# Kernel tuning notes

Hardware: AMD Instinct MI355X
Metric: run time of the kernel (lower is better)

Reference implementation:

```python
import jax, jax.numpy as jnp
import numpy as np

N_NODES = 100000
N_EDGES = 1600000
IN_C, HID_C, OUT_C = 128, 128, 64


def gcn_conv(x, src, dst, W, b, num_nodes):
    # PyG GCNConv: add self-loops, symmetric normalization, linear transform,
    # aggregate source features into targets.
    h = x @ W  # [N, C_out]
    loop = jnp.arange(num_nodes, dtype=src.dtype)
    s = jnp.concatenate([src, loop])
    d = jnp.concatenate([dst, loop])
    deg = jax.ops.segment_sum(jnp.ones_like(d, dtype=h.dtype), d, num_segments=num_nodes)
    inv_sqrt = jnp.where(deg > 0, jax.lax.rsqrt(deg), 0.0)
    norm = inv_sqrt[s] * inv_sqrt[d]  # [E+N]
    msgs = h[s] * norm[:, None]  # gather + scale
    out = jax.ops.segment_sum(msgs, d, num_segments=num_nodes)  # scatter-add
    return out + b


def setup_inputs() -> dict:
    key = jax.random.key(0)
    k1, k2, k3, k4 = jax.random.split(key, 4)
    x = jax.random.normal(k1, (N_NODES, IN_C), dtype=jnp.float32)
    edge_index = jax.random.randint(k2, (2, N_EDGES), 0, N_NODES, dtype=jnp.int64)
    W1 = jax.random.normal(k3, (IN_C, HID_C), dtype=jnp.float32) * (1.0 / np.sqrt(IN_C))
    b1 = jnp.zeros((HID_C,), dtype=jnp.float32)
    W2 = jax.random.normal(k4, (HID_C, OUT_C), dtype=jnp.float32) * (1.0 / np.sqrt(HID_C))
    b2 = jnp.zeros((OUT_C,), dtype=jnp.float32)
    return {"x": x, "edge_index": edge_index, "W1": W1, "b1": b1, "W2": W2, "b2": b2}


def reference(x, edge_index, W1, b1, W2, b2):
    num_nodes = x.shape[0]
    src, dst = edge_index[0], edge_index[1]  # PyG flow: source -> target
    h = gcn_conv(x, src, dst, W1, b1, num_nodes)
    h = jax.nn.relu(h)  # dropout is identity in eval mode
    out = gcn_conv(h, src, dst, W2, b2, num_nodes)
    return out
```

## Files before the change

kernel.cpp:

```cpp
#include <hip/hip_runtime.h>

#define IN_C 128
#define HID_C 128
#define OUT_C 64

#define BSPAN 256
#define BCAP  5120
#define NBMAX 512
#define ACHUNK 4096

typedef unsigned int uint32;
typedef unsigned short ushort16;
typedef _Float16 f16;
typedef f16   f16x8 __attribute__((ext_vector_type(8)));
typedef float f32x4 __attribute__((ext_vector_type(4)));


__device__ __forceinline__ ushort16 f2bf(float f) {
    union { float f; uint32 u; } v; v.f = f;
    uint32 r = v.u + 0x7FFFu + ((v.u >> 16) & 1u);
    return (ushort16)(r >> 16);
}

__device__ __forceinline__ void unpack2(uint32 u, float& f0, float& f1) {
    union { uint32 x; float f; } a, b;
    a.x = u << 16;
    b.x = u & 0xFFFF0000u;
    f0 = a.f; f1 = b.f;
}


__launch_bounds__(256)
__global__ void bin_edges_kernel(const int* __restrict__ src, const int* __restrict__ dst,
                                 int* __restrict__ bucketCur, uint32* __restrict__ binned,
                                 int E, int nbuck) {
    __shared__ int hist[NBMAX];
    __shared__ int base[NBMAX];
    const int tid = threadIdx.x;
    const int e0  = blockIdx.x * ACHUNK;

    for (int i = tid; i < NBMAX; i += 256) hist[i] = 0;
    __syncthreads();

    int d[16], s[16], rk[16];
#pragma unroll
    for (int j = 0; j < 16; j++) {
        int e = e0 + j * 256 + tid;
        if (e < E) {
            d[j] = dst[e];
            s[j] = src[e];
            rk[j] = atomicAdd(&hist[d[j] >> 8], 1);
        } else d[j] = -1;
    }
    __syncthreads();

    for (int b = tid; b < nbuck; b += 256) {
        int h = hist[b];
        base[b] = h ? atomicAdd(&bucketCur[b], h) : 0;
    }
    __syncthreads();

#pragma unroll
    for (int j = 0; j < 16; j++) {
        if (d[j] >= 0) {
            int b = d[j] >> 8;
            int pos = base[b] + rk[j];
            if (pos < BCAP)
                binned[(size_t)b * BCAP + pos] =
                    ((uint32)(d[j] & 255) << 17) | (uint32)s[j];
        }
    }
}


__launch_bounds__(256)
__global__ void bucket_csr_kernel(const uint32* __restrict__ binned,
                                  const int* __restrict__ bucketCur,
                                  int* __restrict__ csr_src, int* __restrict__ rowbeg,
                                  int* __restrict__ rowend, float* __restrict__ inv, int N) {
    constexpr int MAXIT = BCAP / 256;
    __shared__ int cnt[BSPAN];
    __shared__ int scn[BSPAN];
    __shared__ int excl[BSPAN];
    const int b   = blockIdx.x;
    const int tid = threadIdx.x;
    const int n0  = b * BSPAN;
    const int ne  = min(bucketCur[b], BCAP);
    const uint32* bp = binned + (size_t)b * BCAP;

    cnt[tid] = 0;
    __syncthreads();

    uint32 ebuf[MAXIT];
    int    rbuf[MAXIT];
    int nmine = 0;
    for (int i = tid; i < ne; i += 256) {
        uint32 e = bp[i];
        ebuf[nmine] = e;
        rbuf[nmine] = atomicAdd(&cnt[e >> 17], 1);
        nmine++;
    }
    __syncthreads();

    int v = cnt[tid];
    scn[tid] = v;
    __syncthreads();
    for (int off = 1; off < 256; off <<= 1) {
        int u = (tid >= off) ? scn[tid - off] : 0;
        __syncthreads();
        scn[tid] += u;
        __syncthreads();
    }
    int ex = scn[tid] - v;
    excl[tid] = ex;

    int n = n0 + tid;
    if (n < N) {
        int gb = b * BCAP + ex;
        rowbeg[n] = gb;
        rowend[n] = gb + v;
        inv[n] = rsqrtf((float)(v + 1));
    }
    __syncthreads();

    for (int j = 0; j < nmine; j++) {
        uint32 e = ebuf[j];
        csr_src[(size_t)b * BCAP + excl[e >> 17] + rbuf[j]] = (int)(e & 0x1FFFFu);
    }
}


template <int C>
__device__ __forceinline__ void wprep_one(const float* __restrict__ W, f16* __restrict__ Wf, int t) {
    constexpr int NCT = C / 16;
    int lane = t & 63;
    int ctkc = t >> 6;
    int ct = ctkc % NCT, kc = ctkc / NCT;
    int kbase = kc * 32 + (lane >> 4) * 8;
    int col   = ct * 16 + (lane & 15);
    f16 v[8];
#pragma unroll
    for (int j = 0; j < 8; j++) v[j] = (f16)W[(size_t)(kbase + j) * C + col];
    *(uint4*)(Wf + (size_t)t * 8) = *(const uint4*)v;
}

__global__ void wprep_both(const float* __restrict__ W1, f16* __restrict__ Wf1,
                           const float* __restrict__ W2, f16* __restrict__ Wf2) {
    constexpr int T1 = 4 * (HID_C / 16) * 64;
    constexpr int T2 = 4 * (OUT_C / 16) * 64;
    int t = blockIdx.x * 256 + threadIdx.x;
    if (t < T1)            wprep_one<HID_C>(W1, Wf1, t);
    else if (t < T1 + T2)  wprep_one<OUT_C>(W2, Wf2, t - T1);
}


template <int C, bool AF16>
__launch_bounds__(256)
__global__ void mfma_gemm(const void* __restrict__ Xv, const f16* __restrict__ Wf,
                          const float* __restrict__ inv, ushort16* __restrict__ outb, int N) {
    constexpr int NCT = C / 16;
    __shared__ __align__(16) f16 As[4 * 4 * 64 * 8];
    __shared__ __align__(16) f16 Bs[4 * NCT * 64 * 8];

    const int tid  = threadIdx.x;
    const int lane = tid & 63;
    const int w    = tid >> 6;
    const int row0 = blockIdx.x * 64;

    {
        constexpr int TOT = 4 * NCT * 64 * 8;
        const uint4* src = (const uint4*)Wf;
        uint4* dst = (uint4*)Bs;
#pragma unroll
        for (int i = 0; i < TOT / 8 / 256; i++)
            dst[tid + i * 256] = src[tid + i * 256];
    }

    {
        int r   = tid >> 2;
        int seg = tid & 3;
        int row = row0 + r;
        int ws_ = r >> 4;
        int r15 = r & 15;
        if (!AF16) {
            const float* X = (const float*)Xv;
#pragma unroll
            for (int i = 0; i < 8; i++) {
                int k = seg * 32 + i * 4;
                float4 v = make_float4(0.f, 0.f, 0.f, 0.f);
                if (row < N) v = *(const float4*)(X + (size_t)row * 128 + k);
                int q = (k >> 3) & 3, j0 = k & 7;
                f16 h[4] = {(f16)v.x, (f16)v.y, (f16)v.z, (f16)v.w};
                int slot = ((seg * 4 + ws_) * 64 + (q * 16 + r15)) * 8 + j0;
                *(uint2*)(As + slot) = *(const uint2*)h;
            }
        } else {
            const f16* X = (const f16*)Xv;
#pragma unroll
            for (int i = 0; i < 4; i++) {
                int k = seg * 32 + i * 8;
                uint4 v = make_uint4(0, 0, 0, 0);
                if (row < N) v = *(const uint4*)(X + (size_t)row * 128 + k);
                int q = (k >> 3) & 3;
                int slot = ((seg * 4 + ws_) * 64 + (q * 16 + r15)) * 8;
                *(uint4*)(As + slot) = v;
            }
        }
    }
    __syncthreads();

    f32x4 acc[NCT];
#pragma unroll
    for (int c = 0; c < NCT; c++) acc[c] = (f32x4){0.f, 0.f, 0.f, 0.f};

#pragma unroll
    for (int kc = 0; kc < 4; kc++) {
        f16x8 a = *(const f16x8*)&As[((kc * 4 + w) * 64 + lane) * 8];
#pragma unroll
        for (int ct = 0; ct < NCT; ct++) {
            f16x8 b = *(const f16x8*)&Bs[((kc * NCT + ct) * 64 + lane) * 8];
            acc[ct] = __builtin_amdgcn_mfma_f32_16x16x32_f16(a, b, acc[ct], 0, 0, 0);
        }
    }

    __syncthreads();
    ushort16* Ds = (ushort16*)As;
    const int q = lane >> 4;
    float iv[4];
#pragma unroll
    for (int reg = 0; reg < 4; reg++) {
        int row = row0 + w * 16 + q * 4 + reg;
        iv[reg] = (row < N) ? inv[row] : 0.f;
    }
#pragma unroll
    for (int ct = 0; ct < NCT; ct++) {
#pragma unroll
        for (int reg = 0; reg < 4; reg++) {
            int r = w * 16 + q * 4 + reg;
            Ds[r * C + ct * 16 + (lane & 15)] = f2bf(acc[ct][reg] * iv[reg]);
        }
    }
    __syncthreads();
    {
        int r  = tid >> 2;
        int row = row0 + r;
        if (row < N) {
            constexpr int SPT = C / 4;
            int c0 = (tid & 3) * SPT;
            const uint4* s = (const uint4*)&Ds[r * C + c0];
            uint4* d = (uint4*)(outb + (size_t)row * C + c0);
#pragma unroll
            for (int i = 0; i < SPT / 8; i++) d[i] = s[i];
        }
    }
}


__device__ __forceinline__ void acc_row(uint4 r, float* acc) {
    float f0, f1;
    unpack2(r.x, f0, f1); acc[0] += f0; acc[1] += f1;
    unpack2(r.y, f0, f1); acc[2] += f0; acc[3] += f1;
    unpack2(r.z, f0, f1); acc[4] += f0; acc[5] += f1;
    unpack2(r.w, f0, f1); acc[6] += f0; acc[7] += f1;
}

template <int C, bool RELU, bool F16OUT>
__launch_bounds__(256)
__global__ void gather_agg_bf16(const int* __restrict__ rowbeg, const int* __restrict__ rowend,
                                const int* __restrict__ csr_src,
                                const ushort16* __restrict__ hsb, const float* __restrict__ inv,
                                const float* __restrict__ b, void* __restrict__ outv, int N) {
    constexpr int TPN = C / 8;
    constexpr int NPB = 256 / TPN;
    int n    = blockIdx.x * NPB + threadIdx.x / TPN;
    int lane = threadIdx.x % TPN;
    if (n >= N) return;
    int c8 = lane * 8;

    float acc[8];
    {
        uint4 raw = *(const uint4*)(hsb + (size_t)n * C + c8);
        unpack2(raw.x, acc[0], acc[1]);
        unpack2(raw.y, acc[2], acc[3]);
        unpack2(raw.z, acc[4], acc[5]);
        unpack2(raw.w, acc[6], acc[7]);
    }

    int beg = rowbeg[n];
    int end = rowend[n];
    int i = beg;
    for (; i + 4 <= end; i += 4) {
        int s0 = csr_src[i];
        int s1 = csr_src[i + 1];
        int s2 = csr_src[i + 2];
        int s3 = csr_src[i + 3];
        uint4 r0 = *(const uint4*)(hsb + (size_t)s0 * C + c8);
        uint4 r1 = *(const uint4*)(hsb + (size_t)s1 * C + c8);
        uint4 r2 = *(const uint4*)(hsb + (size_t)s2 * C + c8);
        uint4 r3 = *(const uint4*)(hsb + (size_t)s3 * C + c8);
        acc_row(r0, acc); acc_row(r1, acc); acc_row(r2, acc); acc_row(r3, acc);
    }
    for (; i < end; i++) {
        int s0 = csr_src[i];
        uint4 r0 = *(const uint4*)(hsb + (size_t)s0 * C + c8);
        acc_row(r0, acc);
    }

    float iv = inv[n];
    float4 b0 = *(const float4*)(b + c8);
    float4 b1 = *(const float4*)(b + c8 + 4);
    float r[8];
    r[0] = fmaf(iv, acc[0], b0.x); r[1] = fmaf(iv, acc[1], b0.y);
    r[2] = fmaf(iv, acc[2], b0.z); r[3] = fmaf(iv, acc[3], b0.w);
    r[4] = fmaf(iv, acc[4], b1.x); r[5] = fmaf(iv, acc[5], b1.y);
    r[6] = fmaf(iv, acc[6], b1.z); r[7] = fmaf(iv, acc[7], b1.w);
    if (RELU) {
#pragma unroll
        for (int j = 0; j < 8; j++) r[j] = fmaxf(r[j], 0.f);
    }
    if (F16OUT) {
        f16 o[8];
#pragma unroll
        for (int j = 0; j < 8; j++) o[j] = (f16)r[j];
        *(uint4*)((f16*)outv + (size_t)n * C + c8) = *(const uint4*)o;
    } else {
        float* po = (float*)outv + (size_t)n * C + c8;
        *(float4*)(po)     = make_float4(r[0], r[1], r[2], r[3]);
        *(float4*)(po + 4) = make_float4(r[4], r[5], r[6], r[7]);
    }
}

extern "C" void kernel_launch(void* const* d_in, const int* in_sizes, int n_in,
                              void* d_out, int out_size, void* d_ws, size_t ws_size,
                              hipStream_t stream) {
    const float* x  = (const float*)d_in[0];
    const int*   ei = (const int*)d_in[1];
    const float* W1 = (const float*)d_in[2];
    const float* b1 = (const float*)d_in[3];
    const float* W2 = (const float*)d_in[4];
    const float* b2 = (const float*)d_in[5];
    float* out = (float*)d_out;

    const int N = in_sizes[0] / IN_C;
    const int E = in_sizes[1] / 2;
    const int* src = ei;
    const int* dst = ei + E;
    const int nbuck = (N + BSPAN - 1) / BSPAN;

    char* ws = (char*)d_ws;
    auto align_up = [](size_t v) { return (v + 1023) & ~(size_t)1023; };
    size_t off = 0;
    int*      bucketCur = (int*)(ws + off);      off += align_up((size_t)nbuck * sizeof(int));
    float*    inv       = (float*)(ws + off);    off += align_up((size_t)N * sizeof(float));
    int*      rowbeg    = (int*)(ws + off);      off += align_up((size_t)N * sizeof(int));
    int*      rowend    = (int*)(ws + off);      off += align_up((size_t)N * sizeof(int));
    uint32*   binned    = (uint32*)(ws + off);   off += align_up((size_t)nbuck * BCAP * sizeof(uint32));
    int*      csrs      = (int*)(ws + off);      off += align_up((size_t)nbuck * BCAP * sizeof(int));
    f16*      Wf1       = (f16*)(ws + off);      off += align_up((size_t)4 * (HID_C/16) * 64 * 8 * sizeof(f16));
    f16*      Wf2       = (f16*)(ws + off);      off += align_up((size_t)4 * (OUT_C/16) * 64 * 8 * sizeof(f16));
    ushort16* hs1b      = (ushort16*)(ws + off); off += align_up((size_t)N * HID_C * sizeof(ushort16));
    f16*      h1post    = (f16*)(ws + off);      off += align_up((size_t)N * HID_C * sizeof(f16));
    ushort16* hs2b      = (ushort16*)(ws + off); off += align_up((size_t)N * OUT_C * sizeof(ushort16));

    hipMemsetAsync(bucketCur, 0, (size_t)nbuck * sizeof(int), stream);
    wprep_both<<<(4 * (HID_C/16 + OUT_C/16) * 64 + 255) / 256, 256, 0, stream>>>(W1, Wf1, W2, Wf2);
    bin_edges_kernel<<<(E + ACHUNK - 1) / ACHUNK, 256, 0, stream>>>(
        src, dst, bucketCur, binned, E, nbuck);
    bucket_csr_kernel<<<nbuck, 256, 0, stream>>>(
        binned, bucketCur, csrs, rowbeg, rowend, inv, N);

    mfma_gemm<HID_C, false><<<(N + 63) / 64, 256, 0, stream>>>(x, Wf1, inv, hs1b, N);
    {
        constexpr int NPB = 256 / (HID_C / 8);
        gather_agg_bf16<HID_C, true, true><<<(N + NPB - 1) / NPB, 256, 0, stream>>>(
            rowbeg, rowend, csrs, hs1b, inv, b1, h1post, N);
    }

    mfma_gemm<OUT_C, true><<<(N + 63) / 64, 256, 0, stream>>>(h1post, Wf2, inv, hs2b, N);
    {
        constexpr int NPB = 256 / (OUT_C / 8);
        gather_agg_bf16<OUT_C, false, false><<<(N + NPB - 1) / NPB, 256, 0, stream>>>(
            rowbeg, rowend, csrs, hs2b, inv, b2, out, N);
    }
}
```

Measured before the change: 267.8 us.

## Shard hidden features into 8-channel column slices for cache-local gather

The GEMM outputs and the layer-1 aggregated features are now stored channel-group-major: each 8-channel group of all nodes is one contiguous slice. The gather kernel assigns one thread per node per group, and consecutive blocks (blockIdx % NG) cycle through groups, so concurrently running blocks touch slices of about 1.6 MB that can stay resident in L2. The GEMM epilogue stages through padded shared memory (stride C+4) to avoid bank conflicts. The trade-off is that each node's CSR index list is re-read once per group, and every gathered row access is a single 16-byte load rather than part of a coalesced 256-byte row.

```diff
diff --git a/kernel.cpp b/kernel.cpp
--- a/kernel.cpp
+++ b/kernel.cpp
@@ -27,6 +27,14 @@
     a.x = u << 16;
     b.x = u & 0xFFFF0000u;
     f0 = a.f; f1 = b.f;
+}
+
+__device__ __forceinline__ void acc_row(uint4 r, float* acc) {
+    float f0, f1;
+    unpack2(r.x, f0, f1); acc[0] += f0; acc[1] += f1;
+    unpack2(r.y, f0, f1); acc[2] += f0; acc[3] += f1;
+    unpack2(r.z, f0, f1); acc[4] += f0; acc[5] += f1;
+    unpack2(r.w, f0, f1); acc[6] += f0; acc[7] += f1;
 }
 
 
@@ -159,6 +167,8 @@
 __global__ void mfma_gemm(const void* __restrict__ Xv, const f16* __restrict__ Wf,
                           const float* __restrict__ inv, ushort16* __restrict__ outb, int N) {
     constexpr int NCT = C / 16;
+    constexpr int NG  = C / 8;
+    constexpr int SD  = C + 4;
     __shared__ __align__(16) f16 As[4 * 4 * 64 * 8];
     __shared__ __align__(16) f16 Bs[4 * NCT * 64 * 8];
 
@@ -198,11 +208,10 @@
             const f16* X = (const f16*)Xv;
 #pragma unroll
             for (int i = 0; i < 4; i++) {
-                int k = seg * 32 + i * 8;
+                int g = seg * 4 + i;
                 uint4 v = make_uint4(0, 0, 0, 0);
-                if (row < N) v = *(const uint4*)(X + (size_t)row * 128 + k);
-                int q = (k >> 3) & 3;
-                int slot = ((seg * 4 + ws_) * 64 + (q * 16 + r15)) * 8;
+                if (row < N) v = *(const uint4*)(X + ((size_t)g * N + row) * 8);
+                int slot = ((seg * 4 + ws_) * 64 + (i * 16 + r15)) * 8;
                 *(uint4*)(As + slot) = v;
             }
         }
@@ -224,7 +233,7 @@
     }
 
     __syncthreads();
-    ushort16* Ds = (ushort16*)As;
+    ushort16* Ds = (ushort16*)Bs;
     const int q = lane >> 4;
     float iv[4];
 #pragma unroll
@@ -237,49 +246,37 @@
 #pragma unroll
         for (int reg = 0; reg < 4; reg++) {
             int r = w * 16 + q * 4 + reg;
-            Ds[r * C + ct * 16 + (lane & 15)] = f2bf(acc[ct][reg] * iv[reg]);
+            Ds[r * SD + ct * 16 + (lane & 15)] = f2bf(acc[ct][reg] * iv[reg]);
         }
     }
     __syncthreads();
-    {
-        int r  = tid >> 2;
+#pragma unroll
+    for (int it = tid; it < 64 * NG; it += 256) {
+        int r = it & 63, g = it >> 6;
         int row = row0 + r;
-        if (row < N) {
-            constexpr int SPT = C / 4;
-            int c0 = (tid & 3) * SPT;
-            const uint4* s = (const uint4*)&Ds[r * C + c0];
-            uint4* d = (uint4*)(outb + (size_t)row * C + c0);
-#pragma unroll
-            for (int i = 0; i < SPT / 8; i++) d[i] = s[i];
-        }
-    }
-}
-
-
-__device__ __forceinline__ void acc_row(uint4 r, float* acc) {
-    float f0, f1;
-    unpack2(r.x, f0, f1); acc[0] += f0; acc[1] += f1;
-    unpack2(r.y, f0, f1); acc[2] += f0; acc[3] += f1;
-    unpack2(r.z, f0, f1); acc[4] += f0; acc[5] += f1;
-    unpack2(r.w, f0, f1); acc[6] += f0; acc[7] += f1;
-}
+        if (row < N)
+            *(uint4*)(outb + ((size_t)g * N + row) * 8) = *(const uint4*)&Ds[r * SD + g * 8];
+    }
+}
+
 
 template <int C, bool RELU, bool F16OUT>
 __launch_bounds__(256)
-__global__ void gather_agg_bf16(const int* __restrict__ rowbeg, const int* __restrict__ rowend,
-                                const int* __restrict__ csr_src,
-                                const ushort16* __restrict__ hsb, const float* __restrict__ inv,
-                                const float* __restrict__ b, void* __restrict__ outv, int N) {
-    constexpr int TPN = C / 8;
-    constexpr int NPB = 256 / TPN;
-    int n    = blockIdx.x * NPB + threadIdx.x / TPN;
-    int lane = threadIdx.x % TPN;
+__global__ void gather_sharded(const int* __restrict__ rowbeg, const int* __restrict__ rowend,
+                               const int* __restrict__ csr,
+                               const ushort16* __restrict__ hsb,
+                               const float* __restrict__ inv, const float* __restrict__ bias,
+                               void* __restrict__ outv, int N) {
+    constexpr int NG = C / 8;
+    const int g  = blockIdx.x % NG;
+    const int nb = blockIdx.x / NG;
+    const int n  = nb * 256 + threadIdx.x;
     if (n >= N) return;
-    int c8 = lane * 8;
+    const ushort16* slice = hsb + (size_t)g * N * 8;
 
     float acc[8];
     {
-        uint4 raw = *(const uint4*)(hsb + (size_t)n * C + c8);
+        uint4 raw = *(const uint4*)(slice + (size_t)n * 8);
         unpack2(raw.x, acc[0], acc[1]);
         unpack2(raw.y, acc[2], acc[3]);
         unpack2(raw.z, acc[4], acc[5]);
@@ -290,25 +287,24 @@
     int end = rowend[n];
     int i = beg;
     for (; i + 4 <= end; i += 4) {
-        int s0 = csr_src[i];
-        int s1 = csr_src[i + 1];
-        int s2 = csr_src[i + 2];
-        int s3 = csr_src[i + 3];
-        uint4 r0 = *(const uint4*)(hsb + (size_t)s0 * C + c8);
-        uint4 r1 = *(const uint4*)(hsb + (size_t)s1 * C + c8);
-        uint4 r2 = *(const uint4*)(hsb + (size_t)s2 * C + c8);
-        uint4 r3 = *(const uint4*)(hsb + (size_t)s3 * C + c8);
+        int s0 = csr[i];
+        int s1 = csr[i + 1];
+        int s2 = csr[i + 2];
+        int s3 = csr[i + 3];
+        uint4 r0 = *(const uint4*)(slice + (size_t)s0 * 8);
+        uint4 r1 = *(const uint4*)(slice + (size_t)s1 * 8);
+        uint4 r2 = *(const uint4*)(slice + (size_t)s2 * 8);
+        uint4 r3 = *(const uint4*)(slice + (size_t)s3 * 8);
         acc_row(r0, acc); acc_row(r1, acc); acc_row(r2, acc); acc_row(r3, acc);
     }
     for (; i < end; i++) {
-        int s0 = csr_src[i];
-        uint4 r0 = *(const uint4*)(hsb + (size_t)s0 * C + c8);
+        uint4 r0 = *(const uint4*)(slice + (size_t)csr[i] * 8);
         acc_row(r0, acc);
     }
 
     float iv = inv[n];
-    float4 b0 = *(const float4*)(b + c8);
-    float4 b1 = *(const float4*)(b + c8 + 4);
+    float4 b0 = *(const float4*)(bias + g * 8);
+    float4 b1 = *(const float4*)(bias + g * 8 + 4);
     float r[8];
     r[0] = fmaf(iv, acc[0], b0.x); r[1] = fmaf(iv, acc[1], b0.y);
     r[2] = fmaf(iv, acc[2], b0.z); r[3] = fmaf(iv, acc[3], b0.w);
@@ -322,9 +318,9 @@
         f16 o[8];
 #pragma unroll
         for (int j = 0; j < 8; j++) o[j] = (f16)r[j];
-        *(uint4*)((f16*)outv + (size_t)n * C + c8) = *(const uint4*)o;
+        *(uint4*)((f16*)outv + ((size_t)g * N + n) * 8) = *(const uint4*)o;
     } else {
-        float* po = (float*)outv + (size_t)n * C + c8;
+        float* po = (float*)outv + (size_t)n * C + g * 8;
         *(float4*)(po)     = make_float4(r[0], r[1], r[2], r[3]);
         *(float4*)(po + 4) = make_float4(r[4], r[5], r[6], r[7]);
     }
@@ -346,6 +342,7 @@
     const int* src = ei;
     const int* dst = ei + E;
     const int nbuck = (N + BSPAN - 1) / BSPAN;
+    const int nrb   = (N + 255) / 256;
 
     char* ws = (char*)d_ws;
     auto align_up = [](size_t v) { return (v + 1023) & ~(size_t)1023; };
@@ -370,16 +367,10 @@
         binned, bucketCur, csrs, rowbeg, rowend, inv, N);
 
     mfma_gemm<HID_C, false><<<(N + 63) / 64, 256, 0, stream>>>(x, Wf1, inv, hs1b, N);
-    {
-        constexpr int NPB = 256 / (HID_C / 8);
-        gather_agg_bf16<HID_C, true, true><<<(N + NPB - 1) / NPB, 256, 0, stream>>>(
-            rowbeg, rowend, csrs, hs1b, inv, b1, h1post, N);
-    }
+    gather_sharded<HID_C, true, true><<<(HID_C / 8) * nrb, 256, 0, stream>>>(
+        rowbeg, rowend, csrs, hs1b, inv, b1, h1post, N);
 
     mfma_gemm<OUT_C, true><<<(N + 63) / 64, 256, 0, stream>>>(h1post, Wf2, inv, hs2b, N);
-    {
-        constexpr int NPB = 256 / (OUT_C / 8);
-        gather_agg_bf16<OUT_C, false, false><<<(N + NPB - 1) / NPB, 256, 0, stream>>>(
-            rowbeg, rowend, csrs, hs2b, inv, b2, out, N);
-    }
-}
+    gather_sharded<OUT_C, false, false><<<(OUT_C / 8) * nrb, 256, 0, stream>>>(
+        rowbeg, rowend, csrs, hs2b, inv, b2, out, N);
+}
```

Result: slower. 399.1 us (+49.0%).

## Fuse layer-1 aggregation with layer-2 GEMM and fold bucket memset into wprep

Applied to the files above, without the earlier changes.

Layer-1 neighbour aggregation (bias, ReLU) and the layer-2 MFMA GEMM now run in one kernel. Each block gathers 64 nodes into LDS as f16 and multiplies by W2 directly, so the N×128 f16 intermediate is never written to or reread from global memory. The bucket counter memset moves into the weight-prep kernel, removing one launch. In exchange, each thread gathers 32 channels per node with only 4 threads per node, which is less memory-level parallelism than the previous 16 threads per node. It also raises register pressure and may cause load imbalance within a block.

```diff
diff --git a/kernel.cpp b/kernel.cpp
--- a/kernel.cpp
+++ b/kernel.cpp
@@ -27,6 +27,14 @@
     a.x = u << 16;
     b.x = u & 0xFFFF0000u;
     f0 = a.f; f1 = b.f;
+}
+
+__device__ __forceinline__ void acc_row(uint4 r, float* acc) {
+    float f0, f1;
+    unpack2(r.x, f0, f1); acc[0] += f0; acc[1] += f1;
+    unpack2(r.y, f0, f1); acc[2] += f0; acc[3] += f1;
+    unpack2(r.z, f0, f1); acc[4] += f0; acc[5] += f1;
+    unpack2(r.w, f0, f1); acc[6] += f0; acc[7] += f1;
 }
 
 
@@ -145,18 +153,20 @@
 }
 
 __global__ void wprep_both(const float* __restrict__ W1, f16* __restrict__ Wf1,
-                           const float* __restrict__ W2, f16* __restrict__ Wf2) {
+                           const float* __restrict__ W2, f16* __restrict__ Wf2,
+                           int* __restrict__ bucketCur, int nbuck) {
     constexpr int T1 = 4 * (HID_C / 16) * 64;
     constexpr int T2 = 4 * (OUT_C / 16) * 64;
     int t = blockIdx.x * 256 + threadIdx.x;
+    if (t < nbuck) bucketCur[t] = 0;
     if (t < T1)            wprep_one<HID_C>(W1, Wf1, t);
     else if (t < T1 + T2)  wprep_one<OUT_C>(W2, Wf2, t - T1);
 }
 
 
-template <int C, bool AF16>
+template <int C>
 __launch_bounds__(256)
-__global__ void mfma_gemm(const void* __restrict__ Xv, const f16* __restrict__ Wf,
+__global__ void mfma_gemm(const float* __restrict__ X, const f16* __restrict__ Wf,
                           const float* __restrict__ inv, ushort16* __restrict__ outb, int N) {
     constexpr int NCT = C / 16;
     __shared__ __align__(16) f16 As[4 * 4 * 64 * 8];
@@ -182,29 +192,15 @@
         int row = row0 + r;
         int ws_ = r >> 4;
         int r15 = r & 15;
-        if (!AF16) {
-            const float* X = (const float*)Xv;
-#pragma unroll
-            for (int i = 0; i < 8; i++) {
-                int k = seg * 32 + i * 4;
-                float4 v = make_float4(0.f, 0.f, 0.f, 0.f);
-                if (row < N) v = *(const float4*)(X + (size_t)row * 128 + k);
-                int q = (k >> 3) & 3, j0 = k & 7;
-                f16 h[4] = {(f16)v.x, (f16)v.y, (f16)v.z, (f16)v.w};
-                int slot = ((seg * 4 + ws_) * 64 + (q * 16 + r15)) * 8 + j0;
-                *(uint2*)(As + slot) = *(const uint2*)h;
-            }
-        } else {
-            const f16* X = (const f16*)Xv;
-#pragma unroll
-            for (int i = 0; i < 4; i++) {
-                int k = seg * 32 + i * 8;
-                uint4 v = make_uint4(0, 0, 0, 0);
-                if (row < N) v = *(const uint4*)(X + (size_t)row * 128 + k);
-                int q = (k >> 3) & 3;
-                int slot = ((seg * 4 + ws_) * 64 + (q * 16 + r15)) * 8;
-                *(uint4*)(As + slot) = v;
-            }
+#pragma unroll
+        for (int i = 0; i < 8; i++) {
+            int k = seg * 32 + i * 4;
+            float4 v = make_float4(0.f, 0.f, 0.f, 0.f);
+            if (row < N) v = *(const float4*)(X + (size_t)row * 128 + k);
+            int q = (k >> 3) & 3, j0 = k & 7;
+            f16 h[4] = {(f16)v.x, (f16)v.y, (f16)v.z, (f16)v.w};
+            int slot = ((seg * 4 + ws_) * 64 + (q * 16 + r15)) * 8 + j0;
+            *(uint2*)(As + slot) = *(const uint2*)h;
         }
     }
     __syncthreads();
@@ -212,7 +208,6 @@
     f32x4 acc[NCT];
 #pragma unroll
     for (int c = 0; c < NCT; c++) acc[c] = (f32x4){0.f, 0.f, 0.f, 0.f};
-
 #pragma unroll
     for (int kc = 0; kc < 4; kc++) {
         f16x8 a = *(const f16x8*)&As[((kc * 4 + w) * 64 + lane) * 8];
@@ -256,20 +251,142 @@
 }
 
 
-__device__ __forceinline__ void acc_row(uint4 r, float* acc) {
-    float f0, f1;
-    unpack2(r.x, f0, f1); acc[0] += f0; acc[1] += f1;
-    unpack2(r.y, f0, f1); acc[2] += f0; acc[3] += f1;
-    unpack2(r.z, f0, f1); acc[4] += f0; acc[5] += f1;
-    unpack2(r.w, f0, f1); acc[6] += f0; acc[7] += f1;
-}
-
-template <int C, bool RELU, bool F16OUT>
+__launch_bounds__(256)
+__global__ void fused_gather_gemm(const int* __restrict__ rowbeg, const int* __restrict__ rowend,
+                                  const int* __restrict__ csr,
+                                  const ushort16* __restrict__ hsb,
+                                  const float* __restrict__ inv, const float* __restrict__ bias1,
+                                  const f16* __restrict__ Wf2,
+                                  ushort16* __restrict__ outb, int N) {
+    constexpr int CIN = 128, COUT = 64, NCT = COUT / 16;
+    __shared__ __align__(16) f16 As[4 * 4 * 64 * 8];
+    __shared__ __align__(16) f16 Bs[4 * NCT * 64 * 8];
+
+    const int tid  = threadIdx.x;
+    const int lane = tid & 63;
+    const int w    = tid >> 6;
+    const int row0 = blockIdx.x * 64;
+
+    {
+        constexpr int TOT = 4 * NCT * 64 * 8;
+        const uint4* s = (const uint4*)Wf2;
+        uint4* d = (uint4*)Bs;
+#pragma unroll
+        for (int i = 0; i < TOT / 8 / 256; i++)
+            d[tid + i * 256] = s[tid + i * 256];
+    }
+
+    {
+        int r = tid >> 2;
+        int q = tid & 3;
+        int n = row0 + r;
+        float acc[32];
+#pragma unroll
+        for (int j = 0; j < 32; j++) acc[j] = 0.f;
+
+        if (n < N) {
+            const ushort16* base = hsb + (size_t)n * CIN + q * 32;
+            uint4 s0 = *(const uint4*)(base);
+            uint4 s1 = *(const uint4*)(base + 8);
+            uint4 s2 = *(const uint4*)(base + 16);
+            uint4 s3 = *(const uint4*)(base + 24);
+            acc_row(s0, acc); acc_row(s1, acc + 8); acc_row(s2, acc + 16); acc_row(s3, acc + 24);
+
+            int beg = rowbeg[n], end = rowend[n];
+            int i = beg;
+            for (; i + 2 <= end; i += 2) {
+                const ushort16* p0 = hsb + (size_t)csr[i]     * CIN + q * 32;
+                const ushort16* p1 = hsb + (size_t)csr[i + 1] * CIN + q * 32;
+                uint4 a0 = *(const uint4*)(p0);
+                uint4 a1 = *(const uint4*)(p0 + 8);
+                uint4 a2 = *(const uint4*)(p0 + 16);
+                uint4 a3 = *(const uint4*)(p0 + 24);
+                uint4 b0 = *(const uint4*)(p1);
+                uint4 b1 = *(const uint4*)(p1 + 8);
+                uint4 b2 = *(const uint4*)(p1 + 16);
+                uint4 b3 = *(const uint4*)(p1 + 24);
+                acc_row(a0, acc); acc_row(a1, acc + 8); acc_row(a2, acc + 16); acc_row(a3, acc + 24);
+                acc_row(b0, acc); acc_row(b1, acc + 8); acc_row(b2, acc + 16); acc_row(b3, acc + 24);
+            }
+            if (i < end) {
+                const ushort16* p0 = hsb + (size_t)csr[i] * CIN + q * 32;
+                uint4 a0 = *(const uint4*)(p0);
+                uint4 a1 = *(const uint4*)(p0 + 8);
+                uint4 a2 = *(const uint4*)(p0 + 16);
+                uint4 a3 = *(const uint4*)(p0 + 24);
+                acc_row(a0, acc); acc_row(a1, acc + 8); acc_row(a2, acc + 16); acc_row(a3, acc + 24);
+            }
+
+            float iv = inv[n];
+#pragma unroll
+            for (int j = 0; j < 32; j++)
+                acc[j] = fmaxf(fmaf(iv, acc[j], bias1[q * 32 + j]), 0.f);
+        }
+
+        int ws_ = r >> 4, r15 = r & 15;
+#pragma unroll
+        for (int i8 = 0; i8 < 4; i8++) {
+            f16 h[8];
+#pragma unroll
+            for (int j = 0; j < 8; j++) h[j] = (f16)acc[i8 * 8 + j];
+            int slot = ((q * 4 + ws_) * 64 + (i8 * 16 + r15)) * 8;
+            *(uint4*)(As + slot) = *(const uint4*)h;
+        }
+    }
+    __syncthreads();
+
+    f32x4 acc2[NCT];
+#pragma unroll
+    for (int c = 0; c < NCT; c++) acc2[c] = (f32x4){0.f, 0.f, 0.f, 0.f};
+#pragma unroll
+    for (int kc = 0; kc < 4; kc++) {
+        f16x8 a = *(const f16x8*)&As[((kc * 4 + w) * 64 + lane) * 8];
+#pragma unroll
+        for (int ct = 0; ct < NCT; ct++) {
+            f16x8 b = *(const f16x8*)&Bs[((kc * NCT + ct) * 64 + lane) * 8];
+            acc2[ct] = __builtin_amdgcn_mfma_f32_16x16x32_f16(a, b, acc2[ct], 0, 0, 0);
+        }
+    }
+
+    __syncthreads();
+    ushort16* Ds = (ushort16*)As;
+    const int q2 = lane >> 4;
+    float iv2[4];
+#pragma unroll
+    for (int reg = 0; reg < 4; reg++) {
+        int row = row0 + w * 16 + q2 * 4 + reg;
+        iv2[reg] = (row < N) ? inv[row] : 0.f;
+    }
+#pragma unroll
+    for (int ct = 0; ct < NCT; ct++) {
+#pragma unroll
+        for (int reg = 0; reg < 4; reg++) {
+            int r = w * 16 + q2 * 4 + reg;
+            Ds[r * COUT + ct * 16 + (lane & 15)] = f2bf(acc2[ct][reg] * iv2[reg]);
+        }
+    }
+    __syncthreads();
+    {
+        int r   = tid >> 2;
+        int row = row0 + r;
+        if (row < N) {
+            constexpr int SPT = COUT / 4;
+            int c0 = (tid & 3) * SPT;
+            const uint4* s = (const uint4*)&Ds[r * COUT + c0];
+            uint4* d = (uint4*)(outb + (size_t)row * COUT + c0);
+#pragma unroll
+            for (int i = 0; i < SPT / 8; i++) d[i] = s[i];
+        }
+    }
+}
+
+
+template <int C, bool RELU>
 __launch_bounds__(256)
 __global__ void gather_agg_bf16(const int* __restrict__ rowbeg, const int* __restrict__ rowend,
                                 const int* __restrict__ csr_src,
                                 const ushort16* __restrict__ hsb, const float* __restrict__ inv,
-                                const float* __restrict__ b, void* __restrict__ outv, int N) {
+                                const float* __restrict__ b, float* __restrict__ out, int N) {
     constexpr int TPN = C / 8;
     constexpr int NPB = 256 / TPN;
     int n    = blockIdx.x * NPB + threadIdx.x / TPN;
@@ -301,8 +418,7 @@
         acc_row(r0, acc); acc_row(r1, acc); acc_row(r2, acc); acc_row(r3, acc);
     }
     for (; i < end; i++) {
-        int s0 = csr_src[i];
-        uint4 r0 = *(const uint4*)(hsb + (size_t)s0 * C + c8);
+        uint4 r0 = *(const uint4*)(hsb + (size_t)csr_src[i] * C + c8);
         acc_row(r0, acc);
     }
 
@@ -318,16 +434,9 @@
 #pragma unroll
         for (int j = 0; j < 8; j++) r[j] = fmaxf(r[j], 0.f);
     }
-    if (F16OUT) {
-        f16 o[8];
-#pragma unroll
-        for (int j = 0; j < 8; j++) o[j] = (f16)r[j];
-        *(uint4*)((f16*)outv + (size_t)n * C + c8) = *(const uint4*)o;
-    } else {
-        float* po = (float*)outv + (size_t)n * C + c8;
-        *(float4*)(po)     = make_float4(r[0], r[1], r[2], r[3]);
-        *(float4*)(po + 4) = make_float4(r[4], r[5], r[6], r[7]);
-    }
+    float* po = out + (size_t)n * C + c8;
+    *(float4*)(po)     = make_float4(r[0], r[1], r[2], r[3]);
+    *(float4*)(po + 4) = make_float4(r[4], r[5], r[6], r[7]);
 }
 
 extern "C" void kernel_launch(void* const* d_in, const int* in_sizes, int n_in,
@@ -359,27 +468,23 @@
     f16*      Wf1       = (f16*)(ws + off);      off += align_up((size_t)4 * (HID_C/16) * 64 * 8 * sizeof(f16));
     f16*      Wf2       = (f16*)(ws + off);      off += align_up((size_t)4 * (OUT_C/16) * 64 * 8 * sizeof(f16));
     ushort16* hs1b      = (ushort16*)(ws + off); off += align_up((size_t)N * HID_C * sizeof(ushort16));
-    f16*      h1post    = (f16*)(ws + off);      off += align_up((size_t)N * HID_C * sizeof(f16));
     ushort16* hs2b      = (ushort16*)(ws + off); off += align_up((size_t)N * OUT_C * sizeof(ushort16));
 
-    hipMemsetAsync(bucketCur, 0, (size_t)nbuck * sizeof(int), stream);
-    wprep_both<<<(4 * (HID_C/16 + OUT_C/16) * 64 + 255) / 256, 256, 0, stream>>>(W1, Wf1, W2, Wf2);
+    wprep_both<<<(4 * (HID_C/16 + OUT_C/16) * 64 + 255) / 256, 256, 0, stream>>>(
+        W1, Wf1, W2, Wf2, bucketCur, nbuck);
     bin_edges_kernel<<<(E + ACHUNK - 1) / ACHUNK, 256, 0, stream>>>(
         src, dst, bucketCur, binned, E, nbuck);
     bucket_csr_kernel<<<nbuck, 256, 0, stream>>>(
         binned, bucketCur, csrs, rowbeg, rowend, inv, N);
 
-    mfma_gemm<HID_C, false><<<(N + 63) / 64, 256, 0, stream>>>(x, Wf1, inv, hs1b, N);
-    {
-        constexpr int NPB = 256 / (HID_C / 8);
-        gather_agg_bf16<HID_C, true, true><<<(N + NPB - 1) / NPB, 256, 0, stream>>>(
-            rowbeg, rowend, csrs, hs1b, inv, b1, h1post, N);
-    }
-
-    mfma_gemm<OUT_C, true><<<(N + 63) / 64, 256, 0, stream>>>(h1post, Wf2, inv, hs2b, N);
+    mfma_gemm<HID_C><<<(N + 63) / 64, 256, 0, stream>>>(x, Wf1, inv, hs1b, N);
+
+    fused_gather_gemm<<<(N + 63) / 64, 256, 0, stream>>>(
+        rowbeg, rowend, csrs, hs1b, inv, b1, Wf2, hs2b, N);
+
     {
         constexpr int NPB = 256 / (OUT_C / 8);
-        gather_agg_bf16<OUT_C, false, false><<<(N + NPB - 1) / NPB, 256, 0, stream>>>(
+        gather_agg_bf16<OUT_C, false><<<(N + NPB - 1) / NPB, 256, 0, stream>>>(
             rowbeg, rowend, csrs, hs2b, inv, b2, out, N);
     }
 }
```

After: 261.1 us. -2.5%, faster.
